# Kernel tuning notes

Measured on AMD Instinct MI355X. Metric: run time of the kernel, lower is better.

## Reference

```python
import math
import jax, jax.numpy as jnp
import numpy as np

B, T, D, N_SLOTS, TOP_K = 4, 4096, 2048, 4096, 4


def setup_inputs() -> dict:
    key = jax.random.key(0)
    k1, k2, k3, k4, k5 = jax.random.split(key, 5)
    return {
        "x": jax.random.normal(k1, (B, T, D), dtype=jnp.float32),
        "slot_keys": jax.random.normal(k2, (N_SLOTS, D), dtype=jnp.float32) * 0.02,
        "slot_values": jax.random.normal(k3, (N_SLOTS, D), dtype=jnp.float32) * 0.02,
        "Wq": jax.random.normal(k4, (D, D), dtype=jnp.float32) * 0.02,
        "Wout": jax.random.normal(k5, (D, D), dtype=jnp.float32) * 0.02,
        "top_k": TOP_K,
    }


def reference(x, slot_keys, slot_values, Wq, Wout, top_k):
    d = x.shape[-1]
    scale = 1.0 / math.sqrt(d)
    q = jnp.einsum("btd,ed->bte", x, Wq)                 # proj_q (Linear, no bias)
    scores = jnp.einsum("btd,nd->btn", q, slot_keys) * scale  # [B,T,n_slots]
    topk_vals, topk_ids = jax.lax.top_k(scores, top_k)   # [B,T,k]
    attn = jax.nn.softmax(topk_vals, axis=-1)            # [B,T,k]
    gathered = slot_values[topk_ids]                     # [B,T,k,D] gather
    retrieved = jnp.einsum("btk,btkd->btd", attn, gathered)
    return jnp.einsum("btd,ed->bte", retrieved, Wout)    # proj_out
```

## Files before the change

### kernel.cpp

```cpp
#include <hip/hip_runtime.h>
#include <math.h>

#define D_DIM    2048
#define BT_DIM   16384
#define NSLOTS   4096
#define SCALE    0.02209708691207961f
#define MARGIN   0.02f
#define CAND_MAX 16

typedef __attribute__((ext_vector_type(8))) short bf16x8;
typedef __attribute__((ext_vector_type(4))) float f32x4;
typedef __attribute__((ext_vector_type(8))) unsigned short u16x8;
typedef __attribute__((ext_vector_type(4))) unsigned short u16x4;

__device__ __forceinline__ unsigned short f2bf(float f) {
    unsigned int u = __float_as_uint(f);
    return (unsigned short)((u + 0x7fffu + ((u >> 16) & 1u)) >> 16);
}
__device__ __forceinline__ float bf2f(unsigned short s) {
    return __uint_as_float(((unsigned int)s) << 16);
}

__device__ __forceinline__ void async_cp16(const void* g, void* l) {
    __builtin_amdgcn_global_load_lds(
        (const __attribute__((address_space(1))) void*)g,
        (__attribute__((address_space(3))) void*)l, 16, 0, 0);
}

__device__ __forceinline__ bool cand_better(float v, int i, float v2, int i2) {
    return (v > v2) || (v == v2 && i < i2);
}

__device__ __forceinline__ void cand_insert(float v, int idx,
                                            float& v0, int& i0, float& v1, int& i1,
                                            float& v2, int& i2, float& v3, int& i3) {
    if (cand_better(v, idx, v3, i3)) {
        if (cand_better(v, idx, v0, i0)) {
            v3 = v2; i3 = i2; v2 = v1; i2 = i1; v1 = v0; i1 = i0; v0 = v; i0 = idx;
        } else if (cand_better(v, idx, v1, i1)) {
            v3 = v2; i3 = i2; v2 = v1; i2 = i1; v1 = v; i1 = idx;
        } else if (cand_better(v, idx, v2, i2)) {
            v3 = v2; i3 = i2; v2 = v; i2 = idx;
        } else {
            v3 = v; i3 = idx;
        }
    }
}

__device__ __forceinline__ void split3v(float v, unsigned short& h,
                                        unsigned short& m, unsigned short& l) {
    h = f2bf(v);
    const float r1 = v - bf2f(h);
    m = f2bf(r1);
    l = f2bf(r1 - bf2f(m));
}

__global__ __launch_bounds__(256)
void split3_lin(const float* __restrict__ in, unsigned short* __restrict__ oh,
                unsigned short* __restrict__ om, unsigned short* __restrict__ ol) {
    const size_t i = ((size_t)blockIdx.x * 256 + threadIdx.x) * 4;
    const float4 v = *(const float4*)(in + i);
    u16x4 h, m, l;
    unsigned short th, tm, tl;
    split3v(v.x, th, tm, tl); h[0] = th; m[0] = tm; l[0] = tl;
    split3v(v.y, th, tm, tl); h[1] = th; m[1] = tm; l[1] = tl;
    split3v(v.z, th, tm, tl); h[2] = th; m[2] = tm; l[2] = tl;
    split3v(v.w, th, tm, tl); h[3] = th; m[3] = tm; l[3] = tl;
    *(u16x4*)(oh + i) = h;
    *(u16x4*)(om + i) = m;
    *(u16x4*)(ol + i) = l;
}

__global__ __launch_bounds__(256)
void split3_wqT(const float* __restrict__ W, unsigned short* __restrict__ th,
                unsigned short* __restrict__ tm, unsigned short* __restrict__ tl) {
    __shared__ float tile[32][33];
    const int tx  = threadIdx.x & 31;
    const int ty4 = (threadIdx.x >> 5) * 4;
    const int e0  = blockIdx.y * 32;
    const int d0  = blockIdx.x * 32;
#pragma unroll
    for (int r = 0; r < 4; ++r)
        tile[ty4 + r][tx] = W[(size_t)(e0 + ty4 + r) * D_DIM + (d0 + tx)];
    __syncthreads();
#pragma unroll
    for (int r = 0; r < 4; ++r) {
        const float v = tile[tx][ty4 + r];
        unsigned short h, m, l;
        split3v(v, h, m, l);
        const size_t o = (size_t)(d0 + ty4 + r) * D_DIM + (e0 + tx);
        th[o] = h; tm[o] = m; tl[o] = l;
    }
}

__global__ __launch_bounds__(256)
void cvt_f32_bf16(const float* __restrict__ in, unsigned short* __restrict__ out) {
    const size_t i = ((size_t)blockIdx.x * 256 + threadIdx.x) * 8;
    float4 a = *(const float4*)(in + i);
    float4 b = *(const float4*)(in + i + 4);
    u16x8 o;
    o[0] = f2bf(a.x); o[1] = f2bf(a.y); o[2] = f2bf(a.z); o[3] = f2bf(a.w);
    o[4] = f2bf(b.x); o[5] = f2bf(b.y); o[6] = f2bf(b.z); o[7] = f2bf(b.w);
    *(u16x8*)(out + i) = o;
}

__global__ __launch_bounds__(256)
void gemm_kw_mfma6(const unsigned short* __restrict__ Ah,
                   const unsigned short* __restrict__ Am,
                   const unsigned short* __restrict__ Al,
                   const unsigned short* __restrict__ Bh,
                   const unsigned short* __restrict__ Bm,
                   const unsigned short* __restrict__ Bl,
                   float* __restrict__ KW, unsigned short* __restrict__ kwb,
                   int M, int N, int K) {
    __shared__ __align__(16) unsigned short AldsH[128 * 32];
    __shared__ __align__(16) unsigned short AldsM[128 * 32];
    __shared__ __align__(16) unsigned short AldsL[128 * 32];
    __shared__ __align__(16) unsigned short BldsH[128 * 32];
    __shared__ __align__(16) unsigned short BldsM[128 * 32];
    __shared__ __align__(16) unsigned short BldsL[128 * 32];

    const int tid  = threadIdx.x;
    const int lane = tid & 63;
    const int w    = tid >> 6;
    const int wr   = w >> 1, wc = w & 1;
    const int bmr  = blockIdx.y * 128;
    const int bnc  = blockIdx.x * 128;

    const int srow = lane >> 2;
    const int skch = (lane & 3) ^ ((lane >> 3) & 3);
    const int c0 = w, c1 = w + 4;
    size_t oA0 = (size_t)(bmr + c0 * 16 + srow) * K + skch * 8;
    size_t oA1 = (size_t)(bmr + c1 * 16 + srow) * K + skch * 8;
    size_t oB0 = (size_t)(bnc + c0 * 16 + srow) * K + skch * 8;
    size_t oB1 = (size_t)(bnc + c1 * 16 + srow) * K + skch * 8;
    char* lAh0 = (char*)AldsH + c0 * 1024;  char* lAh1 = (char*)AldsH + c1 * 1024;
    char* lAm0 = (char*)AldsM + c0 * 1024;  char* lAm1 = (char*)AldsM + c1 * 1024;
    char* lAl0 = (char*)AldsL + c0 * 1024;  char* lAl1 = (char*)AldsL + c1 * 1024;
    char* lBh0 = (char*)BldsH + c0 * 1024;  char* lBh1 = (char*)BldsH + c1 * 1024;
    char* lBm0 = (char*)BldsM + c0 * 1024;  char* lBm1 = (char*)BldsM + c1 * 1024;
    char* lBl0 = (char*)BldsL + c0 * 1024;  char* lBl1 = (char*)BldsL + c1 * 1024;

    const int kbyte = (((lane >> 4) ^ ((lane >> 1) & 3)) << 4);
    const int rA = wr * 64 + (lane & 15);
    const int rB = wc * 64 + (lane & 15);

    f32x4 acc[4][4] = {};

    for (int kt = 0; kt < K; kt += 32) {
        async_cp16(Ah + oA0, lAh0);  async_cp16(Ah + oA1, lAh1);
        async_cp16(Am + oA0, lAm0);  async_cp16(Am + oA1, lAm1);
        async_cp16(Al + oA0, lAl0);  async_cp16(Al + oA1, lAl1);
        async_cp16(Bh + oB0, lBh0);  async_cp16(Bh + oB1, lBh1);
        async_cp16(Bm + oB0, lBm0);  async_cp16(Bm + oB1, lBm1);
        async_cp16(Bl + oB0, lBl0);  async_cp16(Bl + oB1, lBl1);
        oA0 += 32; oA1 += 32; oB0 += 32; oB1 += 32;
        __syncthreads();

        bf16x8 afh[4], afm[4], afl[4], bfh[4], bfm[4], bfl[4];
#pragma unroll
        for (int i = 0; i < 4; ++i) {
            const int ar = (rA + i * 16) * 64 + kbyte;
            afh[i] = *(const bf16x8*)((const char*)AldsH + ar);
            afm[i] = *(const bf16x8*)((const char*)AldsM + ar);
            afl[i] = *(const bf16x8*)((const char*)AldsL + ar);
            const int br = (rB + i * 16) * 64 + kbyte;
            bfh[i] = *(const bf16x8*)((const char*)BldsH + br);
            bfm[i] = *(const bf16x8*)((const char*)BldsM + br);
            bfl[i] = *(const bf16x8*)((const char*)BldsL + br);
        }
#pragma unroll
        for (int i = 0; i < 4; ++i)
#pragma unroll
            for (int j = 0; j < 4; ++j) {
                f32x4 c = acc[i][j];
                c = __builtin_amdgcn_mfma_f32_16x16x32_bf16(afh[i], bfh[j], c, 0, 0, 0);
                c = __builtin_amdgcn_mfma_f32_16x16x32_bf16(afh[i], bfm[j], c, 0, 0, 0);
                c = __builtin_amdgcn_mfma_f32_16x16x32_bf16(afm[i], bfh[j], c, 0, 0, 0);
                c = __builtin_amdgcn_mfma_f32_16x16x32_bf16(afm[i], bfm[j], c, 0, 0, 0);
                c = __builtin_amdgcn_mfma_f32_16x16x32_bf16(afh[i], bfl[j], c, 0, 0, 0);
                c = __builtin_amdgcn_mfma_f32_16x16x32_bf16(afl[i], bfh[j], c, 0, 0, 0);
                acc[i][j] = c;
            }
        __syncthreads();
    }

    const int orow = (lane >> 4) * 4;
    const int ocol = lane & 15;
#pragma unroll
    for (int i = 0; i < 4; ++i)
#pragma unroll
        for (int j = 0; j < 4; ++j) {
            const size_t base =
                (size_t)(bmr + wr * 64 + i * 16 + orow) * N + (bnc + wc * 64 + j * 16 + ocol);
#pragma unroll
            for (int r = 0; r < 4; ++r) {
                const float v = acc[i][j][r];
                KW[base + (size_t)r * N]  = v;
                kwb[base + (size_t)r * N] = f2bf(v);
            }
        }
}

template <bool BF16_OUT>
__global__ __launch_bounds__(256)
void gemm_bf16_abt(const unsigned short* __restrict__ A,
                   const unsigned short* __restrict__ B,
                   void* __restrict__ Cv, int M, int N, int K) {
    __shared__ __align__(16) unsigned short Alds[128 * 32];
    __shared__ __align__(16) unsigned short Blds[128 * 32];

    const int tid  = threadIdx.x;
    const int lane = tid & 63;
    const int w    = tid >> 6;
    const int wr   = w >> 1, wc = w & 1;
    const int bm   = blockIdx.y * 128;
    const int bn   = blockIdx.x * 128;

    const int srow = lane >> 2;
    const int skch = (lane & 3) ^ ((lane >> 3) & 3);
    const int c0 = w, c1 = w + 4;
    const unsigned short* gA0 = A + (size_t)(bm + c0 * 16 + srow) * K + skch * 8;
    const unsigned short* gA1 = A + (size_t)(bm + c1 * 16 + srow) * K + skch * 8;
    const unsigned short* gB0 = B + (size_t)(bn + c0 * 16 + srow) * K + skch * 8;
    const unsigned short* gB1 = B + (size_t)(bn + c1 * 16 + srow) * K + skch * 8;
    char* lA0 = (char*)Alds + c0 * 1024;
    char* lA1 = (char*)Alds + c1 * 1024;
    char* lB0 = (char*)Blds + c0 * 1024;
    char* lB1 = (char*)Blds + c1 * 1024;

    const int kbyte = (((lane >> 4) ^ ((lane >> 1) & 3)) << 4);
    const int rA = wr * 64 + (lane & 15);
    const int rB = wc * 64 + (lane & 15);

    f32x4 acc[4][4] = {};

    for (int kt = 0; kt < K; kt += 32) {
        async_cp16(gA0, lA0);
        async_cp16(gA1, lA1);
        async_cp16(gB0, lB0);
        async_cp16(gB1, lB1);
        gA0 += 32; gA1 += 32; gB0 += 32; gB1 += 32;
        __syncthreads();

        bf16x8 a[4], b[4];
#pragma unroll
        for (int i = 0; i < 4; ++i) {
            a[i] = *(const bf16x8*)((const char*)Alds + (rA + i * 16) * 64 + kbyte);
            b[i] = *(const bf16x8*)((const char*)Blds + (rB + i * 16) * 64 + kbyte);
        }
#pragma unroll
        for (int i = 0; i < 4; ++i)
#pragma unroll
            for (int j = 0; j < 4; ++j)
                acc[i][j] = __builtin_amdgcn_mfma_f32_16x16x32_bf16(
                    a[i], b[j], acc[i][j], 0, 0, 0);
        __syncthreads();
    }

    const int orow = (lane >> 4) * 4;
    const int ocol = lane & 15;
#pragma unroll
    for (int i = 0; i < 4; ++i)
#pragma unroll
        for (int j = 0; j < 4; ++j) {
            const size_t base =
                (size_t)(bm + wr * 64 + i * 16 + orow) * N + (bn + wc * 64 + j * 16 + ocol);
#pragma unroll
            for (int r = 0; r < 4; ++r) {
                if constexpr (BF16_OUT)
                    ((unsigned short*)Cv)[base + (size_t)r * N] = f2bf(acc[i][j][r]);
                else
                    ((float*)Cv)[base + (size_t)r * N] = acc[i][j][r];
            }
        }
}

__global__ __launch_bounds__(256)
void topk_refine(const unsigned short* __restrict__ scoresb,
                 const float* __restrict__ x,
                 const float* __restrict__ KW,
                 const unsigned short* __restrict__ svb,
                 unsigned short* __restrict__ retr) {
    const int tid  = threadIdx.x;
    const int lane = tid & 63;
    const int w    = tid >> 6;
    const int t    = blockIdx.x * 4 + w;
    const unsigned short* srow = scoresb + (size_t)t * NSLOTS;

    __shared__ int cand[4][CAND_MAX];
    __shared__ int ncand[4];

    unsigned int k[64];
#pragma unroll
    for (int j = 0; j < 8; ++j) {
        const int c0 = j * 512 + lane * 8;
        const u16x8 s8 = *(const u16x8*)(srow + c0);
#pragma unroll
        for (int e = 0; e < 8; ++e) {
            const unsigned int b   = (unsigned int)s8[e] & 0xffffu;
            const unsigned int ord = b ^ ((b & 0x8000u) ? 0xffffu : 0x8000u);
            k[j * 8 + e] = (ord << 12) | (4095u - (unsigned int)(c0 + e));
        }
    }

    unsigned int win[4];
#pragma unroll
    for (int p = 0; p < 4; ++p) {
        unsigned int a16[16];
#pragma unroll
        for (int e = 0; e < 16; ++e)
            a16[e] = max(max(k[e], k[e + 16]), max(k[e + 32], k[e + 48]));
        unsigned int a4[4];
#pragma unroll
        for (int e = 0; e < 4; ++e)
            a4[e] = max(max(a16[e], a16[e + 4]), max(a16[e + 8], a16[e + 12]));
        unsigned int m = max(max(a4[0], a4[1]), max(a4[2], a4[3]));
#pragma unroll
        for (int off = 1; off < 64; off <<= 1)
            m = max(m, (unsigned int)__shfl_xor((int)m, off));
        win[p] = m;
#pragma unroll
        for (int e = 0; e < 64; ++e) k[e] = (k[e] == m) ? 0u : k[e];
    }

    const unsigned int ord3 = win[3] >> 12;
    const unsigned int b3 =
        (ord3 & 0x8000u) ? (ord3 ^ 0x8000u) : (~ord3 & 0xffffu);
    const float thresh = bf2f((unsigned short)b3) - MARGIN;

    if (lane == 0) {
        ncand[w] = 4;
        cand[w][0] = 4095 - (int)(win[0] & 0xfffu);
        cand[w][1] = 4095 - (int)(win[1] & 0xfffu);
        cand[w][2] = 4095 - (int)(win[2] & 0xfffu);
        cand[w][3] = 4095 - (int)(win[3] & 0xfffu);
    }
    __syncthreads();

#pragma unroll
    for (int e = 0; e < 64; ++e) {
        const unsigned int kk  = k[e];
        const unsigned int ordv = kk >> 12;
        const unsigned int bv =
            (ordv & 0x8000u) ? (ordv ^ 0x8000u) : (~ordv & 0xffffu);
        if (bf2f((unsigned short)bv) >= thresh) {
            int p = atomicAdd(&ncand[w], 1);
            if (p < CAND_MAX) cand[w][p] = 4095 - (int)(kk & 0xfffu);
        }
    }
    __syncthreads();
    const int nc = min(ncand[w], CAND_MAX);

    const float* xrow = x + (size_t)t * D_DIM + lane * 4;
    float4 xv[8];
#pragma unroll
    for (int i = 0; i < 8; ++i) xv[i] = *(const float4*)(xrow + 256 * i);

    float r0 = -INFINITY, r1 = -INFINITY, r2 = -INFINITY, r3 = -INFINITY;
    int   q0 = 0x7fffffff, q1 = 0x7fffffff, q2 = 0x7fffffff, q3 = 0x7fffffff;
    for (int c = 0; c < nc; ++c) {
        const int slot = cand[w][c];
        const float* kr = KW + (size_t)slot * D_DIM + lane * 4;
        float p = 0.0f;
#pragma unroll
        for (int i = 0; i < 8; ++i) {
            const float4 k4 = *(const float4*)(kr + 256 * i);
            p = fmaf(xv[i].x, k4.x, p);
            p = fmaf(xv[i].y, k4.y, p);
            p = fmaf(xv[i].z, k4.z, p);
            p = fmaf(xv[i].w, k4.w, p);
        }
#pragma unroll
        for (int off = 1; off < 64; off <<= 1) p += __shfl_xor(p, off);
        cand_insert(p, slot, r0, q0, r1, q1, r2, q2, r3, q3);
    }

    const float e1s = expf(SCALE * (r1 - r0));
    const float e2s = expf(SCALE * (r2 - r0));
    const float e3s = expf(SCALE * (r3 - r0));
    const float inv = 1.0f / (1.0f + e1s + e2s + e3s);
    const float w0s = inv, w1s = e1s * inv, w2s = e2s * inv, w3s = e3s * inv;

    const unsigned short* p0 = svb + (size_t)q0 * D_DIM;
    const unsigned short* p1 = svb + (size_t)q1 * D_DIM;
    const unsigned short* p2 = svb + (size_t)q2 * D_DIM;
    const unsigned short* p3 = svb + (size_t)q3 * D_DIM;
    unsigned short* orow = retr + (size_t)t * D_DIM;
#pragma unroll
    for (int i = 0; i < 4; ++i) {
        const int d0 = lane * 8 + 512 * i;
        u16x8 a0 = *(const u16x8*)(p0 + d0);
        u16x8 a1 = *(const u16x8*)(p1 + d0);
        u16x8 a2 = *(const u16x8*)(p2 + d0);
        u16x8 a3 = *(const u16x8*)(p3 + d0);
        u16x8 o;
#pragma unroll
        for (int e = 0; e < 8; ++e) {
            float s = w0s * bf2f(a0[e]) + w1s * bf2f(a1[e]) +
                      w2s * bf2f(a2[e]) + w3s * bf2f(a3[e]);
            o[e] = f2bf(s);
        }
        *(u16x8*)(orow + d0) = o;
    }
}

extern "C" void kernel_launch(void* const* d_in, const int* in_sizes, int n_in,
                              void* d_out, int out_size, void* d_ws, size_t ws_size,
                              hipStream_t stream) {
    const float* x    = (const float*)d_in[0];
    const float* sk   = (const float*)d_in[1];
    const float* sv   = (const float*)d_in[2];
    const float* wq   = (const float*)d_in[3];
    const float* wout = (const float*)d_in[4];

    char* base = (char*)d_ws;
    unsigned short* scoresb = (unsigned short*)base;
    float*          KW      = (float*)(base + 134217728);
    unsigned short* kwb     = (unsigned short*)(base + 167772160);
    unsigned short* woutb   = (unsigned short*)(base + 184549376);
    unsigned short* xb      = (unsigned short*)(base + 192937984);
    unsigned short* svb     = (unsigned short*)(base + 260046848);
    unsigned short* skh     = (unsigned short*)(base + 293601280);
    unsigned short* skm     = (unsigned short*)(base + 310378496);
    unsigned short* skl     = (unsigned short*)(base + 327155712);
    unsigned short* wqth    = (unsigned short*)(base + 343932928);
    unsigned short* wqtm    = (unsigned short*)(base + 352321536);
    unsigned short* wqtl    = (unsigned short*)(base + 360710144);

    const dim3 blk(256);

    split3_lin<<<dim3((NSLOTS * (size_t)D_DIM) / 1024), blk, 0, stream>>>(
        sk, skh, skm, skl);
    split3_wqT<<<dim3(D_DIM / 32, D_DIM / 32), blk, 0, stream>>>(
        wq, wqth, wqtm, wqtl);

    cvt_f32_bf16<<<dim3((BT_DIM * (size_t)D_DIM) / 2048), blk, 0, stream>>>(x, xb);
    cvt_f32_bf16<<<dim3((D_DIM * (size_t)D_DIM) / 2048), blk, 0, stream>>>(wout, woutb);
    cvt_f32_bf16<<<dim3((NSLOTS * (size_t)D_DIM) / 2048), blk, 0, stream>>>(sv, svb);

    gemm_kw_mfma6<<<dim3(D_DIM / 128, NSLOTS / 128), blk, 0, stream>>>(
        skh, skm, skl, wqth, wqtm, wqtl, KW, kwb, NSLOTS, D_DIM, D_DIM);

    gemm_bf16_abt<true><<<dim3(NSLOTS / 128, BT_DIM / 128), blk, 0, stream>>>(
        xb, kwb, scoresb, BT_DIM, NSLOTS, D_DIM);

    topk_refine<<<dim3(BT_DIM / 4), blk, 0, stream>>>(
        scoresb, x, KW, svb, xb);

    gemm_bf16_abt<false><<<dim3(D_DIM / 128, BT_DIM / 128), blk, 0, stream>>>(
        xb, woutb, (float*)d_out, BT_DIM, D_DIM, D_DIM);
}
```

Before: 989.1 us.

## Precompute slot_values·Woutᵀ and gather projected rows instead of the output GEMM

The output projection is reassociated: slot values are multiplied by Woutᵀ once, a 4096-row GEMM, instead of projecting all 16384 retrieved rows. The top-k kernel then gathers fp32 projected rows and writes the final output directly. This removes most of the FLOPs of the final GEMM. In exchange the gather reads fp32 rows, twice the bytes of the bf16 rows, and the fp32 output is written from the scattered-gather kernel. The SVW buffer reuses workspace that held the split slot keys, which have already been consumed by that point.

New measurement: 892.8 us. 9.7% less time.

```diff
diff --git a/kernel.cpp b/kernel.cpp
--- a/kernel.cpp
+++ b/kernel.cpp
@@ -280,8 +280,8 @@
 void topk_refine(const unsigned short* __restrict__ scoresb,
                  const float* __restrict__ x,
                  const float* __restrict__ KW,
-                 const unsigned short* __restrict__ svb,
-                 unsigned short* __restrict__ retr) {
+                 const float* __restrict__ SVW,
+                 float* __restrict__ out) {
     const int tid  = threadIdx.x;
     const int lane = tid & 63;
     const int w    = tid >> 6;
@@ -382,26 +382,29 @@
     const float inv = 1.0f / (1.0f + e1s + e2s + e3s);
     const float w0s = inv, w1s = e1s * inv, w2s = e2s * inv, w3s = e3s * inv;
 
-    const unsigned short* p0 = svb + (size_t)q0 * D_DIM;
-    const unsigned short* p1 = svb + (size_t)q1 * D_DIM;
-    const unsigned short* p2 = svb + (size_t)q2 * D_DIM;
-    const unsigned short* p3 = svb + (size_t)q3 * D_DIM;
-    unsigned short* orow = retr + (size_t)t * D_DIM;
+    const float* p0 = SVW + (size_t)q0 * D_DIM;
+    const float* p1 = SVW + (size_t)q1 * D_DIM;
+    const float* p2 = SVW + (size_t)q2 * D_DIM;
+    const float* p3 = SVW + (size_t)q3 * D_DIM;
+    float* orow = out + (size_t)t * D_DIM;
 #pragma unroll
     for (int i = 0; i < 4; ++i) {
         const int d0 = lane * 8 + 512 * i;
-        u16x8 a0 = *(const u16x8*)(p0 + d0);
-        u16x8 a1 = *(const u16x8*)(p1 + d0);
-        u16x8 a2 = *(const u16x8*)(p2 + d0);
-        u16x8 a3 = *(const u16x8*)(p3 + d0);
-        u16x8 o;
-#pragma unroll
-        for (int e = 0; e < 8; ++e) {
-            float s = w0s * bf2f(a0[e]) + w1s * bf2f(a1[e]) +
-                      w2s * bf2f(a2[e]) + w3s * bf2f(a3[e]);
-            o[e] = f2bf(s);
-        }
-        *(u16x8*)(orow + d0) = o;
+        float4 a0 = *(const float4*)(p0 + d0), b0 = *(const float4*)(p0 + d0 + 4);
+        float4 a1 = *(const float4*)(p1 + d0), b1 = *(const float4*)(p1 + d0 + 4);
+        float4 a2 = *(const float4*)(p2 + d0), b2 = *(const float4*)(p2 + d0 + 4);
+        float4 a3 = *(const float4*)(p3 + d0), b3v = *(const float4*)(p3 + d0 + 4);
+        float4 oa, ob;
+        oa.x = w0s * a0.x + w1s * a1.x + w2s * a2.x + w3s * a3.x;
+        oa.y = w0s * a0.y + w1s * a1.y + w2s * a2.y + w3s * a3.y;
+        oa.z = w0s * a0.z + w1s * a1.z + w2s * a2.z + w3s * a3.z;
+        oa.w = w0s * a0.w + w1s * a1.w + w2s * a2.w + w3s * a3.w;
+        ob.x = w0s * b0.x + w1s * b1.x + w2s * b2.x + w3s * b3v.x;
+        ob.y = w0s * b0.y + w1s * b1.y + w2s * b2.y + w3s * b3v.y;
+        ob.z = w0s * b0.z + w1s * b1.z + w2s * b2.z + w3s * b3v.z;
+        ob.w = w0s * b0.w + w1s * b1.w + w2s * b2.w + w3s * b3v.w;
+        *(float4*)(orow + d0)     = oa;
+        *(float4*)(orow + d0 + 4) = ob;
     }
 }
 
@@ -427,6 +430,7 @@
     unsigned short* wqth    = (unsigned short*)(base + 343932928);
     unsigned short* wqtm    = (unsigned short*)(base + 352321536);
     unsigned short* wqtl    = (unsigned short*)(base + 360710144);
+    float*          SVW     = (float*)(base + 293601280);
 
     const dim3 blk(256);
 
@@ -442,12 +446,12 @@
     gemm_kw_mfma6<<<dim3(D_DIM / 128, NSLOTS / 128), blk, 0, stream>>>(
         skh, skm, skl, wqth, wqtm, wqtl, KW, kwb, NSLOTS, D_DIM, D_DIM);
 
+    gemm_bf16_abt<false><<<dim3(D_DIM / 128, NSLOTS / 128), blk, 0, stream>>>(
+        svb, woutb, SVW, NSLOTS, D_DIM, D_DIM);
+
     gemm_bf16_abt<true><<<dim3(NSLOTS / 128, BT_DIM / 128), blk, 0, stream>>>(
         xb, kwb, scoresb, BT_DIM, NSLOTS, D_DIM);
 
     topk_refine<<<dim3(BT_DIM / 4), blk, 0, stream>>>(
-        scoresb, x, KW, svb, xb);
-
-    gemm_bf16_abt<false><<<dim3(D_DIM / 128, BT_DIM / 128), blk, 0, stream>>>(
-        xb, woutb, (float*)d_out, BT_DIM, D_DIM, D_DIM);
-}
+        scoresb, x, KW, SVW, (float*)d_out);
+}
```
